# Kernel optimization log

Hardware: AMD Instinct MI355X
Metric: run time of the kernel (lower is better)

Reference implementation:

```python
import jax, jax.numpy as jnp
import numpy as np

N = 262144       # number of samples
DIM = 64         # feature dim
NCLASSES = 128   # number of gaussian classes


def setup_inputs() -> dict:
    key = jax.random.key(0)
    k1, k2, k3, k4 = jax.random.split(key, 4)
    inputs = jax.random.normal(k1, (N, DIM), dtype=jnp.float32)
    target = jax.random.randint(k2, (N,), 0, NCLASSES)
    mean_param = jax.random.normal(k3, (NCLASSES, DIM), dtype=jnp.float32) * 0.02
    cov_param = jax.random.normal(k4, (NCLASSES, DIM, DIM), dtype=jnp.float32) * 0.02
    return {"inputs": inputs, "target": target,
            "mean_param": mean_param, "cov_param": cov_param}


def _l2_distance(sample_mean, sample_cov_sq, mean_param, cov_param):
    # Concrete stand-in for the user-supplied `distance` callable:
    # squared-L2 between the empirical class mean and the learned means,
    # plus the energy of the empirical covariance vector and learned covariances.
    return (jnp.sum((sample_mean[None, :] - mean_param) ** 2)
            + sample_cov_sq
            + jnp.sum(cov_param ** 2))


def reference(inputs, target, mean_param, cov_param):
    nclasses = mean_param.shape[0]
    n = inputs.shape[0]
    # per-class counts and means (fused segmented reduction, one pass)
    counts = jax.ops.segment_sum(jnp.ones((n,), inputs.dtype), target,
                                 num_segments=nclasses)           # [C]
    sums = jax.ops.segment_sum(inputs, target, num_segments=nclasses)  # [C, D]
    means = sums / counts[:, None]                                 # [C, D]
    # center each sample by its class mean  (torch: temp = x - mean)
    temp = inputs - means[target]                                  # [N, D]
    # torch: cov = mm(temp, temp.T).mean(0); row k equals temp_k . mean_j(temp_j)
    # so we only need the per-class sum of centered rows (analytically ~0).
    s = jax.ops.segment_sum(temp, target, num_segments=nclasses)   # [C, D]
    cov = jnp.sum(temp * s[target], axis=-1) / counts[target]      # [N] per-sample entry
    # loss in the python loop is overwritten each iter -> only last class survives
    last = nclasses - 1
    cov_sq_last = jax.ops.segment_sum(cov * cov, target, num_segments=nclasses)[last]
    loss = _l2_distance(means[last], cov_sq_last, mean_param, cov_param)
    return loss
```

## Files before the change

kernel.cpp:

```cpp
#include <hip/hip_runtime.h>


#define DIM 64
#define NCLASSES 128
#define LAST (NCLASSES - 1)
#define NBLOCKS 64

__global__ __launch_bounds__(256) void gem_fused(
    const float* __restrict__ inputs, const int* __restrict__ target,
    const float* __restrict__ mean_param, const float* __restrict__ cov_param,
    int n, int cov_n4, float* __restrict__ ws, float* __restrict__ out)
{
    const int tid  = threadIdx.x;
    const int lane = tid & 63;
    const int wib  = tid >> 6;
    const int gwave = blockIdx.x * 4 + wib;
    const int nwaves = NBLOCKS * 4;

    float acc = 0.f;
    int   cnt = 0;
    for (int cb = gwave * 64; cb < n; cb += nwaves * 64) {
        int t = target[cb + lane];
        unsigned long long m = __ballot(t == LAST);
        cnt += __popcll(m);
        while (m) {
            int b = __ffsll(m) - 1;
            m &= m - 1;
            acc += inputs[(size_t)(cb + b) * DIM + lane];
        }
    }
    __shared__ float sacc[4][DIM];
    __shared__ float sred[4];
    __shared__ int   scnt[4];
    sacc[wib][lane] = acc;
    if (lane == 0) scnt[wib] = cnt;

    const float4* c4 = (const float4*)cov_param;
    float csum = 0.f;
    for (int i = blockIdx.x * 256 + tid; i < cov_n4; i += NBLOCKS * 256) {
        float4 v = c4[i];
        csum += v.x * v.x + v.y * v.y + v.z * v.z + v.w * v.w;
    }
    for (int off = 32; off; off >>= 1) csum += __shfl_down(csum, off, 64);
    if (lane == 0) sred[wib] = csum;
    __syncthreads();

    if (wib == 0) {
        float s = sacc[0][lane] + sacc[1][lane] + sacc[2][lane] + sacc[3][lane];
        atomicAdd(&ws[lane], s);
    }
    if (tid == 0) {
        atomicAdd(&ws[DIM],     (float)(scnt[0] + scnt[1] + scnt[2] + scnt[3]));
        atomicAdd(&ws[DIM + 1], sred[0] + sred[1] + sred[2] + sred[3]);
    }

    __shared__ int amLast;
    __threadfence();
    if (tid == 0) {
        unsigned int old = atomicAdd((unsigned int*)(ws + DIM + 2), 1u);
        amLast = (old == NBLOCKS - 1);
    }
    __syncthreads();
    if (!amLast) return;

    __shared__ float raw[DIM + 2];
    if (tid < DIM + 2) raw[tid] = atomicAdd(&ws[tid], 0.f);
    __syncthreads();

    const float invc = 1.f / raw[DIM];
    float dacc = 0.f;
    for (int i = tid; i < NCLASSES * DIM; i += 256) {
        float d = raw[i & (DIM - 1)] * invc - mean_param[i];
        dacc += d * d;
    }
    for (int off = 32; off; off >>= 1) dacc += __shfl_down(dacc, off, 64);
    __syncthreads();
    if (lane == 0) sred[wib] = dacc;
    __syncthreads();
    if (tid == 0) out[0] = sred[0] + sred[1] + sred[2] + sred[3] + raw[DIM + 1];
}

extern "C" void kernel_launch(void* const* d_in, const int* in_sizes, int n_in,
                              void* d_out, int out_size, void* d_ws, size_t ws_size,
                              hipStream_t stream) {
    const float* inputs     = (const float*)d_in[0];
    const int*   target     = (const int*)d_in[1];
    const float* mean_param = (const float*)d_in[2];
    const float* cov_param  = (const float*)d_in[3];
    float* out = (float*)d_out;
    float* ws  = (float*)d_ws;

    const int n     = in_sizes[0] / DIM;
    const int cov_n = in_sizes[3];

    hipMemsetAsync(d_ws, 0, (DIM + 3) * sizeof(float), stream);
    gem_fused<<<NBLOCKS, 256, 0, stream>>>(inputs, target, mean_param, cov_param,
                                           n, cov_n / 4, ws, out);
}
```

Measured before the change: 117.9 us.

## Raise grid to 128x512 threads and scan targets as int4 per lane

Doubles the block count and block size so 1024 waves scan the target array. Each lane now loads four targets at once with an int4 load, ballots four masks, and gathers the matching input rows, cutting loop iterations per wave. The final reduction precomputes the last-class mean in shared memory and a barrier is added before the completion counter. The trade-off is more blocks contending on the workspace atomics and more divergent gather loops per iteration.

```diff
diff --git a/kernel.cpp b/kernel.cpp
--- a/kernel.cpp
+++ b/kernel.cpp
@@ -4,9 +4,11 @@
 #define DIM 64
 #define NCLASSES 128
 #define LAST (NCLASSES - 1)
-#define NBLOCKS 64
+#define NBLOCKS 128
+#define BLOCK 512
+#define NWAVES (NBLOCKS * 8)
 
-__global__ __launch_bounds__(256) void gem_fused(
+__global__ __launch_bounds__(BLOCK) void gem_fused(
     const float* __restrict__ inputs, const int* __restrict__ target,
     const float* __restrict__ mean_param, const float* __restrict__ cov_param,
     int n, int cov_n4, float* __restrict__ ws, float* __restrict__ out)
@@ -14,48 +16,60 @@
     const int tid  = threadIdx.x;
     const int lane = tid & 63;
     const int wib  = tid >> 6;
-    const int gwave = blockIdx.x * 4 + wib;
-    const int nwaves = NBLOCKS * 4;
+    const int b    = blockIdx.x;
+    const int gwave = b * 8 + wib;
 
     float acc = 0.f;
     int   cnt = 0;
-    for (int cb = gwave * 64; cb < n; cb += nwaves * 64) {
-        int t = target[cb + lane];
-        unsigned long long m = __ballot(t == LAST);
-        cnt += __popcll(m);
-        while (m) {
-            int b = __ffsll(m) - 1;
-            m &= m - 1;
-            acc += inputs[(size_t)(cb + b) * DIM + lane];
+    for (int base = gwave * 256; base < n; base += NWAVES * 256) {
+        const int4 t4 = *(const int4*)(target + base + lane * 4);
+        unsigned long long m0 = __ballot(t4.x == LAST);
+        unsigned long long m1 = __ballot(t4.y == LAST);
+        unsigned long long m2 = __ballot(t4.z == LAST);
+        unsigned long long m3 = __ballot(t4.w == LAST);
+        cnt += __popcll(m0) + __popcll(m1) + __popcll(m2) + __popcll(m3);
+        #pragma unroll
+        for (int j = 0; j < 4; ++j) {
+            unsigned long long m = (j == 0) ? m0 : (j == 1) ? m1 : (j == 2) ? m2 : m3;
+            while (m) {
+                int bit = __ffsll(m) - 1;
+                m &= m - 1;
+                acc += inputs[(size_t)(base + 4 * bit + j) * DIM + lane];
+            }
         }
     }
-    __shared__ float sacc[4][DIM];
-    __shared__ float sred[4];
-    __shared__ int   scnt[4];
-    sacc[wib][lane] = acc;
-    if (lane == 0) scnt[wib] = cnt;
 
     const float4* c4 = (const float4*)cov_param;
     float csum = 0.f;
-    for (int i = blockIdx.x * 256 + tid; i < cov_n4; i += NBLOCKS * 256) {
+    for (int i = b * BLOCK + tid; i < cov_n4; i += NBLOCKS * BLOCK) {
         float4 v = c4[i];
         csum += v.x * v.x + v.y * v.y + v.z * v.z + v.w * v.w;
     }
     for (int off = 32; off; off >>= 1) csum += __shfl_down(csum, off, 64);
-    if (lane == 0) sred[wib] = csum;
+
+    __shared__ float sacc[8][DIM];
+    __shared__ float scov[8];
+    __shared__ int   scnt[8];
+    sacc[wib][lane] = acc;
+    if (lane == 0) { scov[wib] = csum; scnt[wib] = cnt; }
     __syncthreads();
 
     if (wib == 0) {
-        float s = sacc[0][lane] + sacc[1][lane] + sacc[2][lane] + sacc[3][lane];
+        float s = 0.f;
+        #pragma unroll
+        for (int w = 0; w < 8; ++w) s += sacc[w][lane];
         atomicAdd(&ws[lane], s);
     }
     if (tid == 0) {
-        atomicAdd(&ws[DIM],     (float)(scnt[0] + scnt[1] + scnt[2] + scnt[3]));
-        atomicAdd(&ws[DIM + 1], sred[0] + sred[1] + sred[2] + sred[3]);
+        int   c  = 0;   for (int w = 0; w < 8; ++w) c  += scnt[w];
+        float cv = 0.f; for (int w = 0; w < 8; ++w) cv += scov[w];
+        atomicAdd(&ws[DIM],     (float)c);
+        atomicAdd(&ws[DIM + 1], cv);
     }
 
     __shared__ int amLast;
     __threadfence();
+    __syncthreads();
     if (tid == 0) {
         unsigned int old = atomicAdd((unsigned int*)(ws + DIM + 2), 1u);
         amLast = (old == NBLOCKS - 1);
@@ -64,20 +78,27 @@
     if (!amLast) return;
 
     __shared__ float raw[DIM + 2];
+    __shared__ float smean[DIM];
     if (tid < DIM + 2) raw[tid] = atomicAdd(&ws[tid], 0.f);
     __syncthreads();
+    if (tid < DIM) smean[tid] = raw[tid] / raw[DIM];
+    __syncthreads();
 
-    const float invc = 1.f / raw[DIM];
     float dacc = 0.f;
-    for (int i = tid; i < NCLASSES * DIM; i += 256) {
-        float d = raw[i & (DIM - 1)] * invc - mean_param[i];
+    for (int i = tid; i < NCLASSES * DIM; i += BLOCK) {
+        float d = smean[i & (DIM - 1)] - mean_param[i];
         dacc += d * d;
     }
     for (int off = 32; off; off >>= 1) dacc += __shfl_down(dacc, off, 64);
+    __shared__ float fr[8];
+    if (lane == 0) fr[wib] = dacc;
     __syncthreads();
-    if (lane == 0) sred[wib] = dacc;
-    __syncthreads();
-    if (tid == 0) out[0] = sred[0] + sred[1] + sred[2] + sred[3] + raw[DIM + 1];
+    if (tid == 0) {
+        float t = raw[DIM + 1];
+        #pragma unroll
+        for (int w = 0; w < 8; ++w) t += fr[w];
+        out[0] = t;
+    }
 }
 
 extern "C" void kernel_launch(void* const* d_in, const int* in_sizes, int n_in,
@@ -94,6 +115,6 @@
     const int cov_n = in_sizes[3];
 
     hipMemsetAsync(d_ws, 0, (DIM + 3) * sizeof(float), stream);
-    gem_fused<<<NBLOCKS, 256, 0, stream>>>(inputs, target, mean_param, cov_param,
-                                           n, cov_n / 4, ws, out);
+    gem_fused<<<NBLOCKS, BLOCK, 0, stream>>>(inputs, target, mean_param, cov_param,
+                                             n, cov_n / 4, ws, out);
 }
```

After: 116.5 us. No clear change (-1.2%).
